# Kernel optimization log

Hardware: AMD Instinct MI355X
Metric: run time of the kernel (lower is better)

Reference implementation:

```python
import jax, jax.numpy as jnp
import numpy as np
from jax import lax

C = 256
RED = 16
SK = 7  # spatial kernel


def setup_inputs() -> dict:
    key = jax.random.key(0)
    ks = jax.random.split(key, 12)
    b, c, h, w = 4, C, 64, 64
    cr = c // RED
    c8 = c // 8
    s = lambda fan_in: 1.0 / np.sqrt(fan_in)
    return {
        "x": jax.random.normal(ks[0], (b, c, h, w), dtype=jnp.float32),
        # channel MLP (nn.Linear weights are [out, in], no bias)
        "w1": jax.random.normal(ks[1], (cr, c), dtype=jnp.float32) * s(c),
        "w2": jax.random.normal(ks[2], (c, cr), dtype=jnp.float32) * s(cr),
        # spatial conv: [out=1, in=2, 7, 7], no bias
        "w_sp": jax.random.normal(ks[3], (1, 2, SK, SK), dtype=jnp.float32) * s(2 * SK * SK),
        # 1x1 convs (stored as [out, in]) with bias (Conv2d default bias=True)
        "wq": jax.random.normal(ks[4], (c8, c), dtype=jnp.float32) * s(c),
        "bq": jax.random.normal(ks[5], (c8,), dtype=jnp.float32) * s(c),
        "wk": jax.random.normal(ks[6], (c8, c), dtype=jnp.float32) * s(c),
        "bk": jax.random.normal(ks[7], (c8,), dtype=jnp.float32) * s(c),
        "wv": jax.random.normal(ks[8], (c, c), dtype=jnp.float32) * s(c),
        "bv": jax.random.normal(ks[9], (c,), dtype=jnp.float32) * s(c),
        "gamma": jnp.zeros((1,), dtype=jnp.float32),
    }


def reference(x, w1, w2, w_sp, wq, bq, wk, bk, wv, bv, gamma):
    b, c, h, w = x.shape
    hw = h * w

    # ---- channel attention (CBAM) ----
    avg = jnp.mean(x, axis=(2, 3))          # [b, c]
    mx = jnp.max(x, axis=(2, 3))            # [b, c]
    mlp = lambda v: jax.nn.relu(v @ w1.T) @ w2.T
    ch_att = jax.nn.sigmoid(mlp(avg) + mlp(mx))[:, :, None, None]
    x = x * ch_att

    # ---- spatial attention (CBAM) ----
    avg_s = jnp.mean(x, axis=1, keepdims=True)
    max_s = jnp.max(x, axis=1, keepdims=True)
    sp_in = jnp.concatenate([avg_s, max_s], axis=1)  # [b, 2, h, w]
    pad = SK // 2
    sp = lax.conv_general_dilated(
        sp_in, w_sp, window_strides=(1, 1), padding=[(pad, pad), (pad, pad)],
        dimension_numbers=("NCHW", "OIHW", "NCHW"))
    x = x * jax.nn.sigmoid(sp)

    # ---- non-local self-attention (single head, unscaled) ----
    q = jnp.einsum("bchw,oc->bohw", x, wq) + bq[None, :, None, None]
    k = jnp.einsum("bchw,oc->bohw", x, wk) + bk[None, :, None, None]
    v = jnp.einsum("bchw,oc->bohw", x, wv) + bv[None, :, None, None]
    q = q.reshape(b, -1, hw).transpose(0, 2, 1)   # [b, hw, c/8]
    k = k.reshape(b, -1, hw)                      # [b, c/8, hw]
    v = v.reshape(b, c, hw)                       # [b, c, hw]

    attn = jax.nn.softmax(jnp.einsum("bid,bdj->bij", q, k), axis=-1)  # [b, hw, hw]
    out = jnp.einsum("bcj,bij->bci", v, attn).reshape(b, c, h, w)

    return gamma[0] * out + x
```

## Files before the change

### kernel.cpp

```cpp
#include <hip/hip_runtime.h>
#include <math.h>

constexpr int B_  = 4;
constexpr int C_  = 256;
constexpr int HW_ = 4096;
constexpr int CR_ = 16;
constexpr int CQ_ = 32;
constexpr int NAB = 256;

__device__ __forceinline__ float sigmoidf_(float x){ return 1.f/(1.f+expf(-x)); }

__global__ void kA(const float* __restrict__ x, float* __restrict__ avg, float* __restrict__ mxv){
  int bc = blockIdx.x;
  const float4* r4 = (const float4*)(x + (size_t)bc*HW_);
  float s = 0.f, m = -INFINITY;
  #pragma unroll
  for (int i = 0; i < 4; i++){
    float4 v = r4[threadIdx.x + i*256];
    s += v.x+v.y+v.z+v.w;
    m = fmaxf(m, fmaxf(fmaxf(v.x,v.y), fmaxf(v.z,v.w)));
  }
  for (int off = 32; off; off >>= 1){
    s += __shfl_down(s, off);
    m = fmaxf(m, __shfl_down(m, off));
  }
  __shared__ float ss[4], sm[4];
  int w = threadIdx.x >> 6, lane = threadIdx.x & 63;
  if (!lane){ ss[w] = s; sm[w] = m; }
  __syncthreads();
  if (!threadIdx.x){
    avg[bc] = (ss[0]+ss[1]+ss[2]+ss[3]) * (1.f/HW_);
    mxv[bc] = fmaxf(fmaxf(sm[0],sm[1]), fmaxf(sm[2],sm[3]));
  }
}

__global__ void kBC(const float* __restrict__ x,
                    const float* __restrict__ avg, const float* __restrict__ mxv,
                    const float* __restrict__ w1,  const float* __restrict__ w2,
                    float* __restrict__ attg,
                    float* __restrict__ avgs, float* __restrict__ maxs){
  int b = blockIdx.x >> 6, r = blockIdx.x & 63, t = threadIdx.x;
  __shared__ float sa[C_], sm[C_], pa[C_], pm[C_], hs[CR_], satt[C_];
  __shared__ float4 rs[16][16], rm[16][16];
  sa[t] = avg[b*C_+t]; sm[t] = mxv[b*C_+t];
  __syncthreads();
  int h = t >> 4, seg = t & 15;
  float qa = 0.f, qm = 0.f;
  #pragma unroll
  for (int c2 = 0; c2 < 16; c2++){
    int c = seg*16 + c2;
    float ww = w1[h*C_ + c];
    qa += ww*sa[c]; qm += ww*sm[c];
  }
  pa[t] = qa; pm[t] = qm;
  __syncthreads();
  if (t < CR_){
    float ha = 0.f, hm = 0.f;
    #pragma unroll
    for (int s2 = 0; s2 < 16; s2++){ ha += pa[t*16+s2]; hm += pm[t*16+s2]; }
    hs[t] = fmaxf(ha, 0.f) + fmaxf(hm, 0.f);
  }
  __syncthreads();
  float o = 0.f;
  #pragma unroll
  for (int h2 = 0; h2 < CR_; h2++) o += hs[h2]*w2[t*CR_+h2];
  float attv = sigmoidf_(o);
  satt[t] = attv;
  if (r == 0) attg[b*C_+t] = attv;
  __syncthreads();

  int cg = t >> 4, q = t & 15;
  const float4* x4 = (const float4*)x;
  float4 s = {0.f,0.f,0.f,0.f};
  float4 m = {-INFINITY,-INFINITY,-INFINITY,-INFINITY};
  #pragma unroll
  for (int j = 0; j < 16; j++){
    int c = cg*16 + j;
    float a = satt[c];
    float4 v = x4[(size_t)(b*C_+c)*(HW_/4) + (r<<4) + q];
    float vx=v.x*a, vy=v.y*a, vz=v.z*a, vw=v.w*a;
    s.x+=vx; s.y+=vy; s.z+=vz; s.w+=vw;
    m.x=fmaxf(m.x,vx); m.y=fmaxf(m.y,vy); m.z=fmaxf(m.z,vz); m.w=fmaxf(m.w,vw);
  }
  rs[cg][q] = s; rm[cg][q] = m;
  __syncthreads();
  if (t < 16){
    float4 Sv = {0.f,0.f,0.f,0.f};
    float4 Mv = {-INFINITY,-INFINITY,-INFINITY,-INFINITY};
    #pragma unroll
    for (int g2 = 0; g2 < 16; g2++){
      float4 a = rs[g2][t], b2 = rm[g2][t];
      Sv.x+=a.x; Sv.y+=a.y; Sv.z+=a.z; Sv.w+=a.w;
      Mv.x=fmaxf(Mv.x,b2.x); Mv.y=fmaxf(Mv.y,b2.y); Mv.z=fmaxf(Mv.z,b2.z); Mv.w=fmaxf(Mv.w,b2.w);
    }
    Sv.x*=(1.f/C_); Sv.y*=(1.f/C_); Sv.z*=(1.f/C_); Sv.w*=(1.f/C_);
    ((float4*)(avgs + b*HW_ + r*64))[t] = Sv;
    ((float4*)(maxs + b*HW_ + r*64))[t] = Mv;
  }
}

__global__ void kD2s(const float* __restrict__ x, const float* __restrict__ attg,
                     const float* __restrict__ avgs, const float* __restrict__ maxs,
                     const float* __restrict__ wsp, float* __restrict__ out,
                     int* __restrict__ cnt){
  int bx = blockIdx.x;
  int b = bx >> 7, rem = bx & 127, rt = rem >> 3, cp = rem & 7;
  int t = threadIdx.x;
  if (bx == 0 && t == 0) cnt[0] = 0;
  __shared__ float savg[10][64], smax[10][64], ssig[4][64], satt[32], swsp[98];
  if (t < 98) swsp[t] = wsp[t];
  if (t < 32) satt[t] = attg[b*C_ + cp*32 + t];
  for (int idx = t; idx < 640; idx += 256){
    int row = idx >> 6, col = idx & 63;
    int gr = rt*4 - 3 + row;
    float s = 0.f, m = 0.f;
    if ((unsigned)gr < 64u){
      s = avgs[b*HW_ + gr*64 + col];
      m = maxs[b*HW_ + gr*64 + col];
    }
    savg[row][col] = s; smax[row][col] = m;
  }
  __syncthreads();
  int trow = t >> 6, col = t & 63;
  float acc = 0.f;
  #pragma unroll
  for (int ky = 0; ky < 7; ky++){
    #pragma unroll
    for (int kx = 0; kx < 7; kx++){
      int gx = col - 3 + kx;
      if ((unsigned)gx < 64u)
        acc += savg[trow+ky][gx]*swsp[ky*7+kx] + smax[trow+ky][gx]*swsp[49+ky*7+kx];
    }
  }
  ssig[trow][col] = sigmoidf_(acc);
  __syncthreads();
  int f4id = t & 63;
  float4 sg4 = ((const float4*)ssig)[f4id];
  int imgo = rt*64 + f4id;
  const float4* x4 = (const float4*)x;
  float4* o4 = (float4*)out;
  #pragma unroll
  for (int jj = 0; jj < 8; jj++){
    int lc = (t>>6) + jj*4;
    float a = satt[lc];
    size_t g = (size_t)(b*C_ + cp*32 + lc)*(HW_/4) + imgo;
    float4 v = x4[g];
    float4 rr;
    rr.x = v.x*a*sg4.x; rr.y = v.y*a*sg4.y; rr.z = v.z*a*sg4.z; rr.w = v.w*a*sg4.w;
    o4[g] = rr;
  }
}

__global__ void kAttn(const float* __restrict__ gamma, float* __restrict__ out,
                      const float* __restrict__ wq, const float* __restrict__ bq,
                      const float* __restrict__ wk, const float* __restrict__ bk,
                      const float* __restrict__ wv, const float* __restrict__ bv,
                      float* __restrict__ qb, float* __restrict__ kb,
                      float* __restrict__ vb, int* __restrict__ cnt){
  float g = gamma[0];
  if (g == 0.f) return;
  int t = threadIdx.x, bx = blockIdx.x;
  __shared__ union {
    float sx[C_*32];
    struct { float sq[CQ_], red[8], sl[HW_]; } f;
  } S;

  for (int bx2 = bx; bx2 < 512; bx2 += NAB){
    int b2 = bx2 >> 7, tile = bx2 & 127, p0 = tile*32;
    for (int idx = t; idx < C_*32; idx += 256){
      int c = idx >> 5, px = idx & 31;
      S.sx[idx] = out[(size_t)(b2*C_+c)*HW_ + p0 + px];
    }
    __syncthreads();
    for (int oi = t; oi < CQ_*32; oi += 256){
      int o = oi >> 5, px = oi & 31;
      float aq = bq[o], ak = bk[o];
      for (int c = 0; c < C_; c++){ float xv = S.sx[c*32+px]; aq += xv*wq[o*C_+c]; ak += xv*wk[o*C_+c]; }
      qb[(size_t)(b2*CQ_+o)*HW_ + p0 + px] = aq;
      kb[(size_t)(b2*CQ_+o)*HW_ + p0 + px] = ak;
    }
    for (int oi = t; oi < C_*32; oi += 256){
      int o = oi >> 5, px = oi & 31;
      float av = bv[o];
      for (int c = 0; c < C_; c++) av += S.sx[c*32+px]*wv[o*C_+c];
      vb[(size_t)(b2*C_+o)*HW_ + p0 + px] = av;
    }
    __syncthreads();
  }

  __syncthreads();
  if (t == 0){
    __threadfence();
    __hip_atomic_fetch_add(cnt, 1, __ATOMIC_RELEASE, __HIP_MEMORY_SCOPE_AGENT);
    while (__hip_atomic_load(cnt, __ATOMIC_ACQUIRE, __HIP_MEMORY_SCOPE_AGENT) < NAB)
      __builtin_amdgcn_s_sleep(1);
    __threadfence();
  }
  __syncthreads();

  for (int gi = bx; gi < B_*HW_; gi += NAB){
    int b2 = gi >> 12, i = gi & (HW_-1);
    if (t < CQ_) S.f.sq[t] = qb[(size_t)(b2*CQ_+t)*HW_ + i];
    __syncthreads();
    float lmax = -INFINITY;
    for (int j = t; j < HW_; j += 256){
      float l = 0.f;
      for (int d = 0; d < CQ_; d++) l += S.f.sq[d]*kb[(size_t)(b2*CQ_+d)*HW_ + j];
      S.f.sl[j] = l; lmax = fmaxf(lmax, l);
    }
    for (int off = 32; off; off >>= 1) lmax = fmaxf(lmax, __shfl_down(lmax, off));
    if (!(t & 63)) S.f.red[t>>6] = lmax;
    __syncthreads();
    float M = fmaxf(fmaxf(S.f.red[0],S.f.red[1]), fmaxf(S.f.red[2],S.f.red[3]));
    float lsum = 0.f;
    for (int j = t; j < HW_; j += 256){ float p = expf(S.f.sl[j]-M); S.f.sl[j] = p; lsum += p; }
    for (int off = 32; off; off >>= 1) lsum += __shfl_down(lsum, off);
    if (!(t & 63)) S.f.red[4+(t>>6)] = lsum;
    __syncthreads();
    float inv = g/(S.f.red[4]+S.f.red[5]+S.f.red[6]+S.f.red[7]);
    float acc = 0.f;
    const float* vrow = vb + (size_t)(b2*C_+t)*HW_;
    for (int j = 0; j < HW_; j++) acc += S.f.sl[j]*vrow[j];
    out[(size_t)(b2*C_+t)*HW_ + i] += acc*inv;
    __syncthreads();
  }
}

extern "C" void kernel_launch(void* const* d_in, const int* in_sizes, int n_in,
                              void* d_out, int out_size, void* d_ws, size_t ws_size,
                              hipStream_t stream){
  const float* x   = (const float*)d_in[0];
  const float* w1  = (const float*)d_in[1];
  const float* w2  = (const float*)d_in[2];
  const float* wsp = (const float*)d_in[3];
  const float* wq  = (const float*)d_in[4];
  const float* bq  = (const float*)d_in[5];
  const float* wk  = (const float*)d_in[6];
  const float* bk  = (const float*)d_in[7];
  const float* wv  = (const float*)d_in[8];
  const float* bv  = (const float*)d_in[9];
  const float* gm  = (const float*)d_in[10];
  float* out = (float*)d_out;
  float* ws  = (float*)d_ws;

  int*   cnt  = (int*)ws;
  float* avg  = ws + 16;
  float* mxv  = avg  + B_*C_;
  float* attg = mxv  + B_*C_;
  float* avgs = attg + B_*C_;
  float* maxs = avgs + B_*HW_;
  float* qb   = maxs + B_*HW_;
  float* kb   = qb   + B_*CQ_*HW_;
  float* vb   = kb   + B_*CQ_*HW_;
  size_t need_attn = (size_t)((vb + (size_t)B_*C_*HW_) - ws) * sizeof(float);
  (void)in_sizes; (void)n_in; (void)out_size;

  kA  <<<B_*C_, 256, 0, stream>>>(x, avg, mxv);
  kBC <<<256,   256, 0, stream>>>(x, avg, mxv, w1, w2, attg, avgs, maxs);
  kD2s<<<512,   256, 0, stream>>>(x, attg, avgs, maxs, wsp, out, cnt);

  if (ws_size >= need_attn)
    kAttn<<<NAB, 256, 0, stream>>>(gm, out, wq, bq, wk, bk, wv, bv, qb, kb, vb, cnt);
}
```

Before: 105.2 us.

## Fuse spatial-apply and attention kernels into one grid-synced kernel with early x loads

Merges the spatial-attention apply kernel and the self-attention kernel into a single 512-block kernel that uses atomic grid barriers, removing one launch. The counter reset moves into kBC, and shared memory is unioned across the phases. x tiles are loaded into registers at kernel start in both kBC and the fused kernel, so the loads overlap the MLP and conv work. The launch_bounds of (256, 2) with 512 blocks relies on every block being co-resident, and the workspace size check is dropped.

```diff
diff --git a/kernel.cpp b/kernel.cpp
--- a/kernel.cpp
+++ b/kernel.cpp
@@ -6,7 +6,7 @@
 constexpr int HW_ = 4096;
 constexpr int CR_ = 16;
 constexpr int CQ_ = 32;
-constexpr int NAB = 256;
+constexpr int NDB = 512;
 
 __device__ __forceinline__ float sigmoidf_(float x){ return 1.f/(1.f+expf(-x)); }
 
@@ -38,10 +38,19 @@
                     const float* __restrict__ avg, const float* __restrict__ mxv,
                     const float* __restrict__ w1,  const float* __restrict__ w2,
                     float* __restrict__ attg,
-                    float* __restrict__ avgs, float* __restrict__ maxs){
+                    float* __restrict__ avgs, float* __restrict__ maxs,
+                    int* __restrict__ cnt){
   int b = blockIdx.x >> 6, r = blockIdx.x & 63, t = threadIdx.x;
+  if (blockIdx.x == 0 && t == 0) cnt[0] = 0;
   __shared__ float sa[C_], sm[C_], pa[C_], pm[C_], hs[CR_], satt[C_];
   __shared__ float4 rs[16][16], rm[16][16];
+
+  int cg = t >> 4, q = t & 15;
+  const float4* xb = (const float4*)x + (size_t)(b*C_ + cg*16)*(HW_/4) + (r<<4) + q;
+  float4 xv[16];
+  #pragma unroll
+  for (int j = 0; j < 16; j++) xv[j] = xb[(size_t)j*(HW_/4)];
+
   sa[t] = avg[b*C_+t]; sm[t] = mxv[b*C_+t];
   __syncthreads();
   int h = t >> 4, seg = t & 15;
@@ -69,16 +78,12 @@
   if (r == 0) attg[b*C_+t] = attv;
   __syncthreads();
 
-  int cg = t >> 4, q = t & 15;
-  const float4* x4 = (const float4*)x;
   float4 s = {0.f,0.f,0.f,0.f};
   float4 m = {-INFINITY,-INFINITY,-INFINITY,-INFINITY};
   #pragma unroll
   for (int j = 0; j < 16; j++){
-    int c = cg*16 + j;
-    float a = satt[c];
-    float4 v = x4[(size_t)(b*C_+c)*(HW_/4) + (r<<4) + q];
-    float vx=v.x*a, vy=v.y*a, vz=v.z*a, vw=v.w*a;
+    float a = satt[cg*16 + j];
+    float vx=xv[j].x*a, vy=xv[j].y*a, vz=xv[j].z*a, vw=xv[j].w*a;
     s.x+=vx; s.y+=vy; s.z+=vz; s.w+=vw;
     m.x=fmaxf(m.x,vx); m.y=fmaxf(m.y,vy); m.z=fmaxf(m.z,vz); m.w=fmaxf(m.w,vw);
   }
@@ -99,17 +104,38 @@
   }
 }
 
-__global__ void kD2s(const float* __restrict__ x, const float* __restrict__ attg,
-                     const float* __restrict__ avgs, const float* __restrict__ maxs,
-                     const float* __restrict__ wsp, float* __restrict__ out,
-                     int* __restrict__ cnt){
+__global__ void __launch_bounds__(256, 2) kD3(
+    const float* __restrict__ x, const float* __restrict__ attg,
+    const float* __restrict__ avgs, const float* __restrict__ maxs,
+    const float* __restrict__ wsp, const float* __restrict__ gm,
+    const float* __restrict__ wq, const float* __restrict__ bq,
+    const float* __restrict__ wk, const float* __restrict__ bk,
+    const float* __restrict__ wv, const float* __restrict__ bv,
+    float* __restrict__ qb, float* __restrict__ kb, float* __restrict__ vb,
+    float* __restrict__ out, int* __restrict__ cnt){
   int bx = blockIdx.x;
   int b = bx >> 7, rem = bx & 127, rt = rem >> 3, cp = rem & 7;
   int t = threadIdx.x;
-  if (bx == 0 && t == 0) cnt[0] = 0;
-  __shared__ float savg[10][64], smax[10][64], ssig[4][64], satt[32], swsp[98];
-  if (t < 98) swsp[t] = wsp[t];
-  if (t < 32) satt[t] = attg[b*C_ + cp*32 + t];
+  __shared__ union {
+    struct {
+      float savg[10][64], smax[10][64], ssig[4][64], satt[32], swsp[98];
+    } p;
+    float sx[C_*32];
+    struct { float sq[CQ_], red[8], sl[HW_]; } f;
+  } S;
+
+  int f4id = t & 63;
+  int imgo = rt*64 + f4id;
+  const float4* x4 = (const float4*)x;
+  float4 xv[8];
+  {
+    size_t g0 = (size_t)(b*C_ + cp*32 + (t>>6))*(HW_/4) + imgo;
+    #pragma unroll
+    for (int jj = 0; jj < 8; jj++) xv[jj] = x4[g0 + (size_t)jj*4*(HW_/4)];
+  }
+
+  if (t < 98) S.p.swsp[t] = wsp[t];
+  if (t < 32) S.p.satt[t] = attg[b*C_ + cp*32 + t];
   for (int idx = t; idx < 640; idx += 256){
     int row = idx >> 6, col = idx & 63;
     int gr = rt*4 - 3 + row;
@@ -118,7 +144,7 @@
       s = avgs[b*HW_ + gr*64 + col];
       m = maxs[b*HW_ + gr*64 + col];
     }
-    savg[row][col] = s; smax[row][col] = m;
+    S.p.savg[row][col] = s; S.p.smax[row][col] = m;
   }
   __syncthreads();
   int trow = t >> 6, col = t & 63;
@@ -129,44 +155,40 @@
     for (int kx = 0; kx < 7; kx++){
       int gx = col - 3 + kx;
       if ((unsigned)gx < 64u)
-        acc += savg[trow+ky][gx]*swsp[ky*7+kx] + smax[trow+ky][gx]*swsp[49+ky*7+kx];
-    }
-  }
-  ssig[trow][col] = sigmoidf_(acc);
-  __syncthreads();
-  int f4id = t & 63;
-  float4 sg4 = ((const float4*)ssig)[f4id];
-  int imgo = rt*64 + f4id;
-  const float4* x4 = (const float4*)x;
+        acc += S.p.savg[trow+ky][gx]*S.p.swsp[ky*7+kx]
+             + S.p.smax[trow+ky][gx]*S.p.swsp[49+ky*7+kx];
+    }
+  }
+  S.p.ssig[trow][col] = sigmoidf_(acc);
+  __syncthreads();
+  float4 sg4 = ((const float4*)S.p.ssig)[f4id];
   float4* o4 = (float4*)out;
   #pragma unroll
   for (int jj = 0; jj < 8; jj++){
     int lc = (t>>6) + jj*4;
-    float a = satt[lc];
+    float a = S.p.satt[lc];
     size_t g = (size_t)(b*C_ + cp*32 + lc)*(HW_/4) + imgo;
-    float4 v = x4[g];
     float4 rr;
-    rr.x = v.x*a*sg4.x; rr.y = v.y*a*sg4.y; rr.z = v.z*a*sg4.z; rr.w = v.w*a*sg4.w;
+    rr.x = xv[jj].x*a*sg4.x; rr.y = xv[jj].y*a*sg4.y;
+    rr.z = xv[jj].z*a*sg4.z; rr.w = xv[jj].w*a*sg4.w;
     o4[g] = rr;
   }
-}
-
-__global__ void kAttn(const float* __restrict__ gamma, float* __restrict__ out,
-                      const float* __restrict__ wq, const float* __restrict__ bq,
-                      const float* __restrict__ wk, const float* __restrict__ bk,
-                      const float* __restrict__ wv, const float* __restrict__ bv,
-                      float* __restrict__ qb, float* __restrict__ kb,
-                      float* __restrict__ vb, int* __restrict__ cnt){
-  float g = gamma[0];
+
+  float g = gm[0];
   if (g == 0.f) return;
-  int t = threadIdx.x, bx = blockIdx.x;
-  __shared__ union {
-    float sx[C_*32];
-    struct { float sq[CQ_], red[8], sl[HW_]; } f;
-  } S;
-
-  for (int bx2 = bx; bx2 < 512; bx2 += NAB){
-    int b2 = bx2 >> 7, tile = bx2 & 127, p0 = tile*32;
+
+  __syncthreads();
+  if (t == 0){
+    __threadfence();
+    __hip_atomic_fetch_add(cnt, 1, __ATOMIC_RELEASE, __HIP_MEMORY_SCOPE_AGENT);
+    while (__hip_atomic_load(cnt, __ATOMIC_ACQUIRE, __HIP_MEMORY_SCOPE_AGENT) < NDB)
+      __builtin_amdgcn_s_sleep(1);
+    __threadfence();
+  }
+  __syncthreads();
+
+  {
+    int b2 = bx >> 7, tile = bx & 127, p0 = tile*32;
     for (int idx = t; idx < C_*32; idx += 256){
       int c = idx >> 5, px = idx & 31;
       S.sx[idx] = out[(size_t)(b2*C_+c)*HW_ + p0 + px];
@@ -175,7 +197,7 @@
     for (int oi = t; oi < CQ_*32; oi += 256){
       int o = oi >> 5, px = oi & 31;
       float aq = bq[o], ak = bk[o];
-      for (int c = 0; c < C_; c++){ float xv = S.sx[c*32+px]; aq += xv*wq[o*C_+c]; ak += xv*wk[o*C_+c]; }
+      for (int c = 0; c < C_; c++){ float xvv = S.sx[c*32+px]; aq += xvv*wq[o*C_+c]; ak += xvv*wk[o*C_+c]; }
       qb[(size_t)(b2*CQ_+o)*HW_ + p0 + px] = aq;
       kb[(size_t)(b2*CQ_+o)*HW_ + p0 + px] = ak;
     }
@@ -188,17 +210,16 @@
     __syncthreads();
   }
 
-  __syncthreads();
   if (t == 0){
     __threadfence();
     __hip_atomic_fetch_add(cnt, 1, __ATOMIC_RELEASE, __HIP_MEMORY_SCOPE_AGENT);
-    while (__hip_atomic_load(cnt, __ATOMIC_ACQUIRE, __HIP_MEMORY_SCOPE_AGENT) < NAB)
+    while (__hip_atomic_load(cnt, __ATOMIC_ACQUIRE, __HIP_MEMORY_SCOPE_AGENT) < 2*NDB)
       __builtin_amdgcn_s_sleep(1);
     __threadfence();
   }
   __syncthreads();
 
-  for (int gi = bx; gi < B_*HW_; gi += NAB){
+  for (int gi = bx; gi < B_*HW_; gi += NDB){
     int b2 = gi >> 12, i = gi & (HW_-1);
     if (t < CQ_) S.f.sq[t] = qb[(size_t)(b2*CQ_+t)*HW_ + i];
     __syncthreads();
@@ -218,10 +239,10 @@
     if (!(t & 63)) S.f.red[4+(t>>6)] = lsum;
     __syncthreads();
     float inv = g/(S.f.red[4]+S.f.red[5]+S.f.red[6]+S.f.red[7]);
-    float acc = 0.f;
+    float acc2 = 0.f;
     const float* vrow = vb + (size_t)(b2*C_+t)*HW_;
-    for (int j = 0; j < HW_; j++) acc += S.f.sl[j]*vrow[j];
-    out[(size_t)(b2*C_+t)*HW_ + i] += acc*inv;
+    for (int j = 0; j < HW_; j++) acc2 += S.f.sl[j]*vrow[j];
+    out[(size_t)(b2*C_+t)*HW_ + i] += acc2*inv;
     __syncthreads();
   }
 }
@@ -252,13 +273,10 @@
   float* qb   = maxs + B_*HW_;
   float* kb   = qb   + B_*CQ_*HW_;
   float* vb   = kb   + B_*CQ_*HW_;
-  size_t need_attn = (size_t)((vb + (size_t)B_*C_*HW_) - ws) * sizeof(float);
-  (void)in_sizes; (void)n_in; (void)out_size;
-
-  kA  <<<B_*C_, 256, 0, stream>>>(x, avg, mxv);
-  kBC <<<256,   256, 0, stream>>>(x, avg, mxv, w1, w2, attg, avgs, maxs);
-  kD2s<<<512,   256, 0, stream>>>(x, attg, avgs, maxs, wsp, out, cnt);
-
-  if (ws_size >= need_attn)
-    kAttn<<<NAB, 256, 0, stream>>>(gm, out, wq, bq, wk, bk, wv, bv, qb, kb, vb, cnt);
-}
+  (void)in_sizes; (void)n_in; (void)out_size; (void)ws_size;
+
+  kA <<<B_*C_, 256, 0, stream>>>(x, avg, mxv);
+  kBC<<<256,   256, 0, stream>>>(x, avg, mxv, w1, w2, attg, avgs, maxs, cnt);
+  kD3<<<NDB,   256, 0, stream>>>(x, attg, avgs, maxs, wsp, gm,
+                                 wq, bq, wk, bk, wv, bv, qb, kb, vb, out, cnt);
+}
```

Result: no change. 103.5 us, median of 2 (-1.6%).
